# Kernel tuning notes

Hardware: AMD Instinct MI355X
Metric: run time of the kernel (lower is better)

## Reference

```python
import jax, jax.numpy as jnp
import numpy as np


def setup_inputs() -> dict:
    key = jax.random.key(0)
    x = jax.random.normal(key, (524288, 256), dtype=jnp.float32)
    return {"x": x}


def reference(x) -> jnp.ndarray:
    # Original builds diag(1/sqrt(diag(x^T x))) and multiplies: equivalent to
    # dividing each column by its L2 norm. Avoid the O(n*d^2) Gram matrix.
    col_sq_norm = jnp.sum(x * x, axis=0)  # [d]
    return x * jax.lax.rsqrt(col_sq_norm)  # broadcast over rows
```

## Files before the change

kernel.cpp:

```cpp
#include <hip/hip_runtime.h>

#define D   256
#define D4  64

__global__ __launch_bounds__(256) void colsq_partial(
    const float4* __restrict__ x4, float* __restrict__ part,
    int rows, int rows_per_block) {
    __shared__ float4 red[256];
    const int t  = threadIdx.x;
    const int cg = t & 63;
    const int ro = t >> 6;
    const int r0 = blockIdx.x * rows_per_block;
    const int r1 = min(r0 + rows_per_block, rows);

    float4 acc = make_float4(0.f, 0.f, 0.f, 0.f);
    for (int r = r0 + ro; r < r1; r += 4) {
        float4 v = x4[(size_t)r * D4 + cg];
        acc.x += v.x * v.x;
        acc.y += v.y * v.y;
        acc.z += v.z * v.z;
        acc.w += v.w * v.w;
    }
    red[t] = acc;
    __syncthreads();
    if (t < 64) {
        float4 a = red[t];
        float4 b = red[t + 64];
        float4 c = red[t + 128];
        float4 d = red[t + 192];
        float4 s = make_float4(a.x + b.x + c.x + d.x,
                               a.y + b.y + c.y + d.y,
                               a.z + b.z + c.z + d.z,
                               a.w + b.w + c.w + d.w);
        float4* p4 = (float4*)part;
        p4[(size_t)blockIdx.x * D4 + t] = s;
    }
}

__global__ __launch_bounds__(256) void reduce_inv(
    const float* __restrict__ part, float* __restrict__ inv, int nb) {
    __shared__ double red[4][256];
    const int g = blockIdx.x;
    const int t = threadIdx.x;
    const float4* part4 = (const float4*)part;

    double sx = 0.0, sy = 0.0, sz = 0.0, sw = 0.0;
    for (int b = t; b < nb; b += 256) {
        float4 v = part4[(size_t)b * D4 + g];
        sx += (double)v.x; sy += (double)v.y;
        sz += (double)v.z; sw += (double)v.w;
    }
    red[0][t] = sx; red[1][t] = sy; red[2][t] = sz; red[3][t] = sw;
    __syncthreads();
    for (int ofs = 128; ofs > 0; ofs >>= 1) {
        if (t < ofs) {
            red[0][t] += red[0][t + ofs];
            red[1][t] += red[1][t + ofs];
            red[2][t] += red[2][t + ofs];
            red[3][t] += red[3][t + ofs];
        }
        __syncthreads();
    }
    if (t < 4) inv[g * 4 + t] = (float)(1.0 / sqrt(red[t][0]));
}

__global__ __launch_bounds__(256) void scale_cols(
    const float4* __restrict__ x4, const float* __restrict__ inv,
    float4* __restrict__ out4, size_t n4) {
    __shared__ float sinv[D];
    if (threadIdx.x < D) sinv[threadIdx.x] = inv[threadIdx.x];
    __syncthreads();
    const size_t stride = (size_t)gridDim.x * blockDim.x;
    for (size_t i = (size_t)blockIdx.x * blockDim.x + threadIdx.x; i < n4; i += stride) {
        float4 v = x4[i];
        const float4 s = ((const float4*)sinv)[i & 63];
        out4[i] = make_float4(v.x * s.x, v.y * s.y, v.z * s.z, v.w * s.w);
    }
}

extern "C" void kernel_launch(void* const* d_in, const int* in_sizes, int n_in,
                              void* d_out, int out_size, void* d_ws, size_t ws_size,
                              hipStream_t stream) {
    const float* x = (const float*)d_in[0];
    float* out = (float*)d_out;
    const size_t n = (size_t)in_sizes[0];
    const int rows = (int)(n / D);

    int nb = 2048;
    while (nb > 64 && ((size_t)nb * D + D) * sizeof(float) > ws_size) nb >>= 1;

    float* part = (float*)d_ws;
    float* inv  = part + (size_t)nb * D;

    const int rows_per_block = (rows + nb - 1) / nb;

    colsq_partial<<<nb, 256, 0, stream>>>((const float4*)x, part, rows, rows_per_block);
    reduce_inv<<<D4, 256, 0, stream>>>(part, inv, nb);
    scale_cols<<<2048, 256, 0, stream>>>((const float4*)x, inv, (float4*)out, n / 4);
}
```

Baseline: 336.0 us.

## Scale rows in reverse block order with nontemporal loads/stores for cache reuse

Measured after the change: 287.0 us. 1.17x faster.

```diff
diff --git a/kernel.cpp b/kernel.cpp
--- a/kernel.cpp
+++ b/kernel.cpp
@@ -3,37 +3,28 @@
 #define D   256
 #define D4  64
 
+typedef float f4 __attribute__((ext_vector_type(4)));
+
 __global__ __launch_bounds__(256) void colsq_partial(
-    const float4* __restrict__ x4, float* __restrict__ part,
+    const f4* __restrict__ x4, float* __restrict__ part,
     int rows, int rows_per_block) {
-    __shared__ float4 red[256];
+    __shared__ f4 red[256];
     const int t  = threadIdx.x;
     const int cg = t & 63;
     const int ro = t >> 6;
     const int r0 = blockIdx.x * rows_per_block;
     const int r1 = min(r0 + rows_per_block, rows);
 
-    float4 acc = make_float4(0.f, 0.f, 0.f, 0.f);
+    f4 acc = (f4)0.f;
     for (int r = r0 + ro; r < r1; r += 4) {
-        float4 v = x4[(size_t)r * D4 + cg];
-        acc.x += v.x * v.x;
-        acc.y += v.y * v.y;
-        acc.z += v.z * v.z;
-        acc.w += v.w * v.w;
+        f4 v = x4[(size_t)r * D4 + cg];
+        acc += v * v;
     }
     red[t] = acc;
     __syncthreads();
     if (t < 64) {
-        float4 a = red[t];
-        float4 b = red[t + 64];
-        float4 c = red[t + 128];
-        float4 d = red[t + 192];
-        float4 s = make_float4(a.x + b.x + c.x + d.x,
-                               a.y + b.y + c.y + d.y,
-                               a.z + b.z + c.z + d.z,
-                               a.w + b.w + c.w + d.w);
-        float4* p4 = (float4*)part;
-        p4[(size_t)blockIdx.x * D4 + t] = s;
+        f4 s = red[t] + red[t + 64] + red[t + 128] + red[t + 192];
+        ((f4*)part)[(size_t)blockIdx.x * D4 + t] = s;
     }
 }
 
@@ -42,11 +33,11 @@
     __shared__ double red[4][256];
     const int g = blockIdx.x;
     const int t = threadIdx.x;
-    const float4* part4 = (const float4*)part;
+    const f4* part4 = (const f4*)part;
 
     double sx = 0.0, sy = 0.0, sz = 0.0, sw = 0.0;
     for (int b = t; b < nb; b += 256) {
-        float4 v = part4[(size_t)b * D4 + g];
+        f4 v = part4[(size_t)b * D4 + g];
         sx += (double)v.x; sy += (double)v.y;
         sz += (double)v.z; sw += (double)v.w;
     }
@@ -65,16 +56,26 @@
 }
 
 __global__ __launch_bounds__(256) void scale_cols(
-    const float4* __restrict__ x4, const float* __restrict__ inv,
-    float4* __restrict__ out4, size_t n4) {
+    const f4* __restrict__ x4, const float* __restrict__ inv,
+    f4* __restrict__ out4, int rows, int rows_per_block) {
     __shared__ float sinv[D];
     if (threadIdx.x < D) sinv[threadIdx.x] = inv[threadIdx.x];
     __syncthreads();
-    const size_t stride = (size_t)gridDim.x * blockDim.x;
-    for (size_t i = (size_t)blockIdx.x * blockDim.x + threadIdx.x; i < n4; i += stride) {
-        float4 v = x4[i];
-        const float4 s = ((const float4*)sinv)[i & 63];
-        out4[i] = make_float4(v.x * s.x, v.y * s.y, v.z * s.z, v.w * s.w);
+    const int t  = threadIdx.x;
+    const int cg = t & 63;
+    const int ro = t >> 6;
+    const int r0 = blockIdx.x * rows_per_block;
+    const int r1 = min(r0 + rows_per_block, rows);
+    const f4 s = ((const f4*)sinv)[cg];
+
+    const int nq = (r1 - r0 + 3) >> 2;
+    for (int k = nq - 1; k >= 0; --k) {
+        const int r = r0 + k * 4 + ro;
+        if (r < r1) {
+            const size_t idx = (size_t)r * D4 + cg;
+            f4 v = __builtin_nontemporal_load(&x4[idx]);
+            __builtin_nontemporal_store(v * s, &out4[idx]);
+        }
     }
 }
 
@@ -94,7 +95,7 @@
 
     const int rows_per_block = (rows + nb - 1) / nb;
 
-    colsq_partial<<<nb, 256, 0, stream>>>((const float4*)x, part, rows, rows_per_block);
+    colsq_partial<<<nb, 256, 0, stream>>>((const f4*)x, part, rows, rows_per_block);
     reduce_inv<<<D4, 256, 0, stream>>>(part, inv, nb);
-    scale_cols<<<2048, 256, 0, stream>>>((const float4*)x, inv, (float4*)out, n / 4);
+    scale_cols<<<nb, 256, 0, stream>>>((const f4*)x, inv, (f4*)out, rows, rows_per_block);
 }
```
